# Kernel optimization log

Measured on AMD Instinct MI355X. Metric: run time of the kernel, lower is better.

Reference implementation:

```python
import jax, jax.numpy as jnp
import numpy as np

H = 768
NH = 12
HD = H // NH

def _layernorm(x, g, b, eps=1e-5):
    mu = jnp.mean(x, axis=-1, keepdims=True)
    var = jnp.var(x, axis=-1, keepdims=True)
    return (x - mu) * jax.lax.rsqrt(var + eps) * g + b

def setup_inputs() -> dict:
    key = jax.random.key(0)
    ks = jax.random.split(key, 16)
    s = 0.02
    inp = {
        "x": jax.random.normal(ks[0], (2, 2048, H), jnp.float32),
        "t": jax.random.normal(ks[1], (2, 1, H), jnp.float32),
        # MHA params
        "w_qkv": jax.random.normal(ks[2], (H, 3 * H), jnp.float32) * s,
        "b_qkv": jnp.zeros((3 * H,), jnp.float32),
        "w_mffn1": jax.random.normal(ks[3], (H, 4 * H), jnp.float32) * s,
        "b_mffn1": jnp.zeros((4 * H,), jnp.float32),
        "w_mffn2": jax.random.normal(ks[4], (4 * H, H), jnp.float32) * s,
        "b_mffn2": jnp.zeros((H,), jnp.float32),
        # scale_shift (adaLN) params
        "w_ss1": jax.random.normal(ks[5], (H, 6 * H), jnp.float32) * s,
        "b_ss1": jnp.zeros((6 * H,), jnp.float32),
        "w_ss2": jax.random.normal(ks[6], (6 * H, 6 * H), jnp.float32) * s,
        "b_ss2": jnp.zeros((6 * H,), jnp.float32),
        # layernorms
        "ln1_g": jnp.ones((H,), jnp.float32),
        "ln1_b": jnp.zeros((H,), jnp.float32),
        "ln2_g": jnp.ones((H,), jnp.float32),
        "ln2_b": jnp.zeros((H,), jnp.float32),
        # DiT block FFN
        "w_ffn1": jax.random.normal(ks[7], (H, 4 * H), jnp.float32) * s,
        "b_ffn1": jnp.zeros((4 * H,), jnp.float32),
        "w_ffn2": jax.random.normal(ks[8], (4 * H, H), jnp.float32) * s,
        "b_ffn2": jnp.zeros((H,), jnp.float32),
    }
    return inp

def _mha(x, w_qkv, b_qkv, w1, b1, w2, b2):
    B, T, _ = x.shape
    qkv = x @ w_qkv + b_qkv                      # [B,T,3H]
    qkv = qkv.reshape(B, T, 3, NH, HD)           # split (n h s) as in rearrange
    q, k, v = [jnp.transpose(qkv[:, :, i], (0, 2, 1, 3)) for i in range(3)]  # [B,NH,T,HD]
    # NOTE: faithful to source: scale by 1/sqrt(hidden_size), not head_dim
    wei = jnp.einsum('bhtd,bhsd->bhts', q, k) / jnp.sqrt(jnp.asarray(H, x.dtype))
    wei = jax.nn.softmax(wei, axis=-1)           # [B,NH,T,T] (dropout p=0)
    o = jnp.einsum('bhts,bhsd->bhtd', wei, v)    # [B,NH,T,HD]
    o = jnp.transpose(o, (0, 2, 1, 3)).reshape(B, T, H)
    o = jax.nn.gelu(o @ w1 + b1, approximate=False) @ w2 + b2
    return o

def reference(x, t, w_qkv, b_qkv, w_mffn1, b_mffn1, w_mffn2, b_mffn2,
              w_ss1, b_ss1, w_ss2, b_ss2, ln1_g, ln1_b, ln2_g, ln2_b,
              w_ffn1, b_ffn1, w_ffn2, b_ffn2):
    t_emb = jax.nn.silu(t @ w_ss1 + b_ss1) @ w_ss2 + b_ss2   # [B,1,6H]
    g1, be1, a1, g2, be2, a2 = jnp.split(t_emb, 6, axis=-1)  # each [B,1,H]
    residual = x
    h = g1 * _layernorm(x, ln1_g, ln1_b) + be1
    h = _mha(h, w_qkv, b_qkv, w_mffn1, b_mffn1, w_mffn2, b_mffn2)
    x = residual + a1 * h
    residual = x
    h = g2 * _layernorm(x, ln2_g, ln2_b) + be2
    h = jax.nn.gelu(h @ w_ffn1 + b_ffn1, approximate=False) @ w_ffn2 + b_ffn2
    x = residual + a2 * h
    return x
```

## Files before the change

kernel.cpp:

```cpp
#include <hip/hip_runtime.h>
#include <hip/hip_bf16.h>
#include <cstdint>

typedef __bf16 bf16x8 __attribute__((ext_vector_type(8)));
typedef float f32x4 __attribute__((ext_vector_type(4)));

#define SCALE_Q_LOG2E 0.052058770734702875f

__device__ inline float fast_exp2(float x) { return __builtin_amdgcn_exp2f(x); }

struct PrepArgs {
  const float* src[5];
  __hip_bfloat16* dst[5];
  int K[5], N[5];
  int start[6];
  const float* tin;
  const float* w_ss1;
  float* tacc1;
};

__global__ void k_prep(PrepArgs pa) {
  __shared__ float tile[32][33];
  int bid = blockIdx.x;
  int tid = threadIdx.x;
  if (bid < pa.start[5]) {
    int i = 0;
#pragma unroll
    for (int j = 1; j < 5; ++j)
      if (bid >= pa.start[j]) i = j;
    int t0 = bid - pa.start[i];
    int N = pa.N[i], K = pa.K[i];
    int ntx = N >> 5;
    int bx = t0 % ntx, by = t0 / ntx;
    const float* src = pa.src[i];
    __hip_bfloat16* dst = pa.dst[i];
    int n0 = bx * 32, k0 = by * 32;
    int tx = tid & 31, ty = tid >> 5;
#pragma unroll
    for (int r = 0; r < 32; r += 8)
      tile[ty + r][tx] = src[(size_t)(k0 + ty + r) * N + n0 + tx];
    __syncthreads();
#pragma unroll
    for (int r = 0; r < 32; r += 8)
      dst[(size_t)(n0 + ty + r) * K + k0 + tx] = __float2bfloat16(tile[tx][ty + r]);
  } else {
    int t0 = bid - pa.start[5];
    int nb = t0 % 18, kb0 = (t0 / 18) * 64;
    int n = nb * 256 + tid;
    float a0 = 0.f, a1 = 0.f;
    for (int k = kb0; k < kb0 + 64; ++k) {
      float w = pa.w_ss1[(size_t)k * 4608 + n];
      a0 += pa.tin[k] * w;
      a1 += pa.tin[768 + k] * w;
    }
    atomicAdd(&pa.tacc1[n], a0);
    atomicAdd(&pa.tacc1[4608 + n], a1);
  }
}

__global__ void k_tvec2_silu(const float* __restrict__ tacc1, const float* __restrict__ bss1,
                             const float* __restrict__ W, float* __restrict__ teacc) {
  int n = blockIdx.x * 256 + threadIdx.x;
  int kb = blockIdx.y * 64;
  float a0 = 0.f, a1 = 0.f;
  for (int k = kb; k < kb + 64; ++k) {
    float w = W[(size_t)k * 4608 + n];
    float bs = bss1[k];
    float t0 = tacc1[k] + bs;
    float t1 = tacc1[4608 + k] + bs;
    t0 = t0 / (1.f + expf(-t0));
    t1 = t1 / (1.f + expf(-t1));
    a0 += t0 * w;
    a1 += t1 * w;
  }
  atomicAdd(&teacc[n], a0);
  atomicAdd(&teacc[4608 + n], a1);
}

__global__ void k_ln_mod(const float* __restrict__ x, const float* __restrict__ lng,
                         const float* __restrict__ lnb, const float* __restrict__ teacc,
                         const float* __restrict__ bss2,
                         int gofs, int bofs, __hip_bfloat16* __restrict__ out) {
  int row = blockIdx.x;
  int b = row >> 11;
  const float* xr = x + (size_t)row * 768;
  int tid = threadIdx.x;
  float v[3];
  float s = 0.f, sq = 0.f;
#pragma unroll
  for (int i = 0; i < 3; ++i) { v[i] = xr[tid + 256 * i]; s += v[i]; sq += v[i] * v[i]; }
#pragma unroll
  for (int o = 32; o > 0; o >>= 1) { s += __shfl_xor(s, o); sq += __shfl_xor(sq, o); }
  __shared__ float rs[4], rq[4];
  int w = tid >> 6, lane = tid & 63;
  if (lane == 0) { rs[w] = s; rq[w] = sq; }
  __syncthreads();
  s = rs[0] + rs[1] + rs[2] + rs[3];
  sq = rq[0] + rq[1] + rq[2] + rq[3];
  float mu = s * (1.f / 768.f);
  float var = sq * (1.f / 768.f) - mu * mu;
  float rstd = rsqrtf(var + 1e-5f);
  const float* tb = teacc + (size_t)b * 4608;
#pragma unroll
  for (int i = 0; i < 3; ++i) {
    int n = tid + 256 * i;
    float gv = tb[gofs + n] + bss2[gofs + n];
    float bv = tb[bofs + n] + bss2[bofs + n];
    float h = (v[i] - mu) * rstd * lng[n] + lnb[n];
    h = gv * h + bv;
    out[(size_t)row * 768 + n] = __float2bfloat16(h);
  }
}

template <int BM, int BN, int EPI>
__global__ __launch_bounds__(256)
void k_gemm(const __hip_bfloat16* __restrict__ A,
            const __hip_bfloat16* __restrict__ Bt,
            const float* __restrict__ bias,
            float* __restrict__ outF, __hip_bfloat16* __restrict__ outB,
            __hip_bfloat16* __restrict__ outV,
            const float* __restrict__ res, const float* __restrict__ teacc,
            const float* __restrict__ bss2,
            int gofs, int M, int N, int K) {
  constexpr int MI = BM / 32;
  constexpr int NI = BN / 32;
  __shared__ __align__(16) __hip_bfloat16 As[BM * 64];
  __shared__ __align__(16) __hip_bfloat16 Bs[BN * 64];
  const int tid = threadIdx.x;
  const int w = tid >> 6, lane = tid & 63;
  const int quad = lane >> 4, l16 = lane & 15;
  const int wm = w & 1, wn = w >> 1;
  const int m0 = blockIdx.y * BM, n0 = blockIdx.x * BN;
  const int srow = lane >> 3;
  const int sco = ((lane & 7) ^ srow) * 8;

  f32x4 acc[MI][NI] = {};

  for (int k0 = 0; k0 < K; k0 += 64) {
#pragma unroll
    for (int ii = 0; ii < BM / 32; ++ii) {
      int is = w * (BM / 32) + ii;
      const __hip_bfloat16* g = A + (size_t)(m0 + is * 8 + srow) * K + k0 + sco;
      __builtin_amdgcn_global_load_lds(
          (const __attribute__((address_space(1))) void*)g,
          (__attribute__((address_space(3))) void*)&As[is * 512], 16, 0, 0);
    }
#pragma unroll
    for (int ii = 0; ii < BN / 32; ++ii) {
      int is = w * (BN / 32) + ii;
      const __hip_bfloat16* g = Bt + (size_t)(n0 + is * 8 + srow) * K + k0 + sco;
      __builtin_amdgcn_global_load_lds(
          (const __attribute__((address_space(1))) void*)g,
          (__attribute__((address_space(3))) void*)&Bs[is * 512], 16, 0, 0);
    }
    __syncthreads();
#pragma unroll
    for (int ks = 0; ks < 2; ++ks) {
      bf16x8 af[MI], bfv[NI];
#pragma unroll
      for (int i = 0; i < MI; ++i) {
        int row = wm * (BM / 2) + i * 16 + l16;
        int cph = (ks * 4 + quad) ^ (row & 7);
        af[i] = *(const bf16x8*)&As[row * 64 + cph * 8];
      }
#pragma unroll
      for (int j = 0; j < NI; ++j) {
        int row = wn * (BN / 2) + j * 16 + l16;
        int cph = (ks * 4 + quad) ^ (row & 7);
        bfv[j] = *(const bf16x8*)&Bs[row * 64 + cph * 8];
      }
#pragma unroll
      for (int i = 0; i < MI; ++i)
#pragma unroll
        for (int j = 0; j < NI; ++j)
          acc[i][j] = __builtin_amdgcn_mfma_f32_16x16x32_bf16(af[i], bfv[j], acc[i][j], 0, 0, 0);
    }
    __syncthreads();
  }

#pragma unroll
  for (int j = 0; j < NI; ++j) {
    int col = n0 + wn * (BN / 2) + j * 16 + l16;
    float bs = bias[col];
#pragma unroll
    for (int i = 0; i < MI; ++i) {
      int row0 = m0 + wm * (BM / 2) + i * 16 + quad * 4;
      if (EPI == 3 && col >= 1536) {
        int d = col - 1536;
        int nh = d >> 6, dl = d & 63;
        int bb = row0 >> 11, tok = row0 & 2047;
        __hip_bfloat16 tmp[4];
#pragma unroll
        for (int r = 0; r < 4; ++r) tmp[r] = __float2bfloat16(acc[i][j][r] + bs);
        *(uint2*)&outV[((size_t)(bb * 12 + nh) * 64 + dl) * 2048 + tok] = *(uint2*)tmp;
      } else {
#pragma unroll
        for (int r = 0; r < 4; ++r) {
          int row = row0 + r;
          float v = acc[i][j][r] + bs;
          size_t idx = (size_t)row * N + col;
          if (EPI == 0) {
            outF[idx] = v;
          } else if (EPI == 1) {
            float v2 = v * v;
            float u = v * (0.79788456080286536f + 0.035677408136300125f * v2);
            float e = fast_exp2(u * 2.8853900817779268f);
            float gl = v - v * __builtin_amdgcn_rcpf(e + 1.f);
            outB[idx] = __float2bfloat16(gl);
          } else if (EPI == 2) {
            float gate = teacc[(size_t)(row >> 11) * 4608 + gofs + col] + bss2[gofs + col];
            outF[idx] = res[idx] + gate * v;
          } else {
            float vq = (col < 768) ? v * SCALE_Q_LOG2E : v;
            outB[idx] = __float2bfloat16(vq);
          }
        }
      }
    }
  }
}

__launch_bounds__(256)
__global__ void k_attn(const __hip_bfloat16* __restrict__ qkvb,
                       const __hip_bfloat16* __restrict__ VT,
                       __hip_bfloat16* __restrict__ out) {
  __shared__ __align__(16) __hip_bfloat16 Ks[128 * 64];
  __shared__ __align__(16) __hip_bfloat16 Vs[64 * 128];
  __shared__ __align__(16) __hip_bfloat16 Pw[4][16 * 128];

  const int tid = threadIdx.x;
  const int w = tid >> 6, lane = tid & 63;
  const int quad = lane >> 4, l16 = lane & 15;
  const int qt = blockIdx.x, nh = blockIdx.y, b = blockIdx.z;
  const int bh = b * 12 + nh;

  const int qrow0 = b * 2048 + qt * 64 + w * 16;
  bf16x8 qf[2];
#pragma unroll
  for (int t = 0; t < 2; ++t)
    qf[t] = *(const bf16x8*)(qkvb + (size_t)(qrow0 + l16) * 2304 + nh * 64 + t * 32 + quad * 8);

  bf16x8 ones;
#pragma unroll
  for (int j = 0; j < 8; ++j) ones[j] = (__bf16)1.0f;

  f32x4 o[4] = {};
  f32x4 o_l = {};

  const int srow8 = lane >> 3;
  const int sco8 = ((lane & 7) ^ srow8) * 8;
  const int srow4 = lane >> 4;

  for (int kt = 0; kt < 16; ++kt) {
    __syncthreads();
#pragma unroll
    for (int ii = 0; ii < 4; ++ii) {
      int i = w * 4 + ii;
      const __hip_bfloat16* gk =
          qkvb + (size_t)(b * 2048 + kt * 128 + i * 8 + srow8) * 2304 + 768 + nh * 64 + sco8;
      __builtin_amdgcn_global_load_lds(
          (const __attribute__((address_space(1))) void*)gk,
          (__attribute__((address_space(3))) void*)&Ks[i * 512], 16, 0, 0);
      int vrow = i * 4 + srow4;
      const __hip_bfloat16* gv =
          VT + (size_t)(bh * 64 + vrow) * 2048 + kt * 128 + (((lane & 15) ^ (vrow & 15)) * 8);
      __builtin_amdgcn_global_load_lds(
          (const __attribute__((address_space(1))) void*)gv,
          (__attribute__((address_space(3))) void*)&Vs[i * 512], 16, 0, 0);
    }
    __syncthreads();

    f32x4 s_acc[8] = {};
#pragma unroll
    for (int t = 0; t < 2; ++t) {
#pragma unroll
      for (int c = 0; c < 8; ++c) {
        int row = c * 16 + l16;
        int cph = (t * 4 + quad) ^ (row & 7);
        bf16x8 kf = *(const bf16x8*)&Ks[row * 64 + cph * 8];
        s_acc[c] = __builtin_amdgcn_mfma_f32_16x16x32_bf16(qf[t], kf, s_acc[c], 0, 0, 0);
      }
    }

#pragma unroll
    for (int c = 0; c < 8; ++c) {
      int chunk = c * 2 + (l16 >> 3);
#pragma unroll
      for (int r = 0; r < 4; ++r) {
        float p = fast_exp2(s_acc[c][r]);
        int row = quad * 4 + r;
        int phys = chunk ^ row;
        Pw[w][row * 128 + phys * 8 + (l16 & 7)] = __float2bfloat16(p);
      }
    }

#pragma unroll
    for (int t2 = 0; t2 < 4; ++t2) {
      int phys_p = ((t2 * 4 + quad) ^ l16);
      bf16x8 pa = *(const bf16x8*)&Pw[w][l16 * 128 + phys_p * 8];
#pragma unroll
      for (int nf = 0; nf < 4; ++nf) {
        int row = nf * 16 + l16;
        int cph = (t2 * 4 + quad) ^ (row & 15);
        bf16x8 vf = *(const bf16x8*)&Vs[row * 128 + cph * 8];
        o[nf] = __builtin_amdgcn_mfma_f32_16x16x32_bf16(pa, vf, o[nf], 0, 0, 0);
      }
      o_l = __builtin_amdgcn_mfma_f32_16x16x32_bf16(pa, ones, o_l, 0, 0, 0);
    }
  }

  {
    float inv[4];
#pragma unroll
    for (int r = 0; r < 4; ++r) inv[r] = 1.f / o_l[r];
#pragma unroll
    for (int nf = 0; nf < 4; ++nf)
#pragma unroll
      for (int r = 0; r < 4; ++r) {
        int row = qrow0 + quad * 4 + r;
        out[(size_t)row * 768 + nh * 64 + nf * 16 + l16] = __float2bfloat16(o[nf][r] * inv[r]);
      }
  }
}

extern "C" void kernel_launch(void* const* d_in, const int* in_sizes, int n_in,
                              void* d_out, int out_size, void* d_ws, size_t ws_size,
                              hipStream_t stream) {
  const float* x      = (const float*)d_in[0];
  const float* t      = (const float*)d_in[1];
  const float* w_qkv  = (const float*)d_in[2];
  const float* b_qkv  = (const float*)d_in[3];
  const float* w_m1   = (const float*)d_in[4];
  const float* b_m1   = (const float*)d_in[5];
  const float* w_m2   = (const float*)d_in[6];
  const float* b_m2   = (const float*)d_in[7];
  const float* w_ss1  = (const float*)d_in[8];
  const float* b_ss1  = (const float*)d_in[9];
  const float* w_ss2  = (const float*)d_in[10];
  const float* b_ss2  = (const float*)d_in[11];
  const float* ln1_g  = (const float*)d_in[12];
  const float* ln1_b  = (const float*)d_in[13];
  const float* ln2_g  = (const float*)d_in[14];
  const float* ln2_b  = (const float*)d_in[15];
  const float* w_f1   = (const float*)d_in[16];
  const float* b_f1   = (const float*)d_in[17];
  const float* w_f2   = (const float*)d_in[18];
  const float* b_f2   = (const float*)d_in[19];
  float* out = (float*)d_out;

  char* ws = (char*)d_ws;
  size_t off = 0;
  auto alloc = [&](size_t bytes) -> char* {
    off = (off + 255) & ~(size_t)255;
    char* p = ws + off;
    off += bytes;
    return p;
  };
  __hip_bfloat16* wtq  = (__hip_bfloat16*)alloc((size_t)2304 * 768 * 2);
  __hip_bfloat16* wtm1 = (__hip_bfloat16*)alloc((size_t)3072 * 768 * 2);
  __hip_bfloat16* wtm2 = (__hip_bfloat16*)alloc((size_t)768 * 3072 * 2);
  __hip_bfloat16* wtf1 = (__hip_bfloat16*)alloc((size_t)3072 * 768 * 2);
  __hip_bfloat16* wtf2 = (__hip_bfloat16*)alloc((size_t)768 * 3072 * 2);
  float* tacc1 = (float*)alloc(9216 * 4);
  float* teacc = (float*)alloc(9216 * 4);
  __hip_bfloat16* h1   = (__hip_bfloat16*)alloc((size_t)4096 * 768 * 2);
  __hip_bfloat16* qkvb = (__hip_bfloat16*)alloc((size_t)4096 * 2304 * 2);
  __hip_bfloat16* VT   = (__hip_bfloat16*)alloc((size_t)24 * 64 * 2048 * 2);
  __hip_bfloat16* attn = (__hip_bfloat16*)alloc((size_t)4096 * 768 * 2);
  __hip_bfloat16* act1 = (__hip_bfloat16*)alloc((size_t)4096 * 3072 * 2);
  float* x1            = (float*)alloc((size_t)4096 * 768 * 4);

  (void)hipMemsetAsync(tacc1, 0, 9216 * 4, stream);
  (void)hipMemsetAsync(teacc, 0, 9216 * 4, stream);

  PrepArgs pa;
  pa.src[0] = w_qkv; pa.dst[0] = wtq;  pa.K[0] = 768;  pa.N[0] = 2304;
  pa.src[1] = w_m1;  pa.dst[1] = wtm1; pa.K[1] = 768;  pa.N[1] = 3072;
  pa.src[2] = w_m2;  pa.dst[2] = wtm2; pa.K[2] = 3072; pa.N[2] = 768;
  pa.src[3] = w_f1;  pa.dst[3] = wtf1; pa.K[3] = 768;  pa.N[3] = 3072;
  pa.src[4] = w_f2;  pa.dst[4] = wtf2; pa.K[4] = 3072; pa.N[4] = 768;
  pa.start[0] = 0;
  pa.start[1] = pa.start[0] + (2304 / 32) * (768 / 32);
  pa.start[2] = pa.start[1] + (3072 / 32) * (768 / 32);
  pa.start[3] = pa.start[2] + (768 / 32) * (3072 / 32);
  pa.start[4] = pa.start[3] + (3072 / 32) * (768 / 32);
  pa.start[5] = pa.start[4] + (768 / 32) * (3072 / 32);
  pa.tin = t; pa.w_ss1 = w_ss1; pa.tacc1 = tacc1;
  int tvec1_blocks = 18 * 12;
  k_prep<<<pa.start[5] + tvec1_blocks, 256, 0, stream>>>(pa);

  k_tvec2_silu<<<dim3(4608 / 256, 4608 / 64), 256, 0, stream>>>(tacc1, b_ss1, w_ss2, teacc);

  k_ln_mod<<<4096, 256, 0, stream>>>(x, ln1_g, ln1_b, teacc, b_ss2, 0, 768, h1);
  k_gemm<64, 128, 3><<<dim3(2304 / 128, 4096 / 64), 256, 0, stream>>>(
      h1, wtq, b_qkv, nullptr, qkvb, VT, nullptr, nullptr, nullptr, 0, 4096, 2304, 768);
  k_attn<<<dim3(32, 12, 2), 256, 0, stream>>>(qkvb, VT, attn);
  k_gemm<128, 128, 1><<<dim3(3072 / 128, 4096 / 128), 256, 0, stream>>>(
      attn, wtm1, b_m1, nullptr, act1, nullptr, nullptr, nullptr, nullptr, 0, 4096, 3072, 768);
  k_gemm<64, 128, 2><<<dim3(768 / 128, 4096 / 64), 256, 0, stream>>>(
      act1, wtm2, b_m2, x1, nullptr, nullptr, x, teacc, b_ss2, 1536, 4096, 768, 3072);

  k_ln_mod<<<4096, 256, 0, stream>>>(x1, ln2_g, ln2_b, teacc, b_ss2, 2304, 3072, h1);
  k_gemm<128, 128, 1><<<dim3(3072 / 128, 4096 / 128), 256, 0, stream>>>(
      h1, wtf1, b_f1, nullptr, act1, nullptr, nullptr, nullptr, nullptr, 0, 4096, 3072, 768);
  k_gemm<64, 128, 2><<<dim3(768 / 128, 4096 / 64), 256, 0, stream>>>(
      act1, wtf2, b_f2, out, nullptr, nullptr, x1, teacc, b_ss2, 3840, 4096, 768, 3072);
}
```

Measured before the change: 483.4 us.

## Double-buffer K tiles in attention and reuse K buffer for P

The attention kernel now prefetches the next K tile into a second LDS buffer while the current tile is being computed. V is still loaded each iteration but is waited on separately through fine-grained vmcnt counts and raw s_barrier calls, so the V load overlaps the QK^T MFMAs. The separate P scratch array is removed, and P is written into the consumed K buffer, which keeps LDS use roughly flat. It also raises wave priority around the MFMA sections with s_setprio. The risk is that the hand-written waitcnt counts must exactly match the number of outstanding loads, or the kernel reads stale data.

```diff
diff --git a/kernel.cpp b/kernel.cpp
--- a/kernel.cpp
+++ b/kernel.cpp
@@ -224,9 +224,8 @@
 __global__ void k_attn(const __hip_bfloat16* __restrict__ qkvb,
                        const __hip_bfloat16* __restrict__ VT,
                        __hip_bfloat16* __restrict__ out) {
-  __shared__ __align__(16) __hip_bfloat16 Ks[128 * 64];
+  __shared__ __align__(16) __hip_bfloat16 Ks[2][128 * 64];
   __shared__ __align__(16) __hip_bfloat16 Vs[64 * 128];
-  __shared__ __align__(16) __hip_bfloat16 Pw[4][16 * 128];
 
   const int tid = threadIdx.x;
   const int w = tid >> 6, lane = tid & 63;
@@ -239,6 +238,7 @@
 #pragma unroll
   for (int t = 0; t < 2; ++t)
     qf[t] = *(const bf16x8*)(qkvb + (size_t)(qrow0 + l16) * 2304 + nh * 64 + t * 32 + quad * 8);
+  asm volatile("s_waitcnt vmcnt(0)" ::: "memory");
 
   bf16x8 ones;
 #pragma unroll
@@ -251,16 +251,26 @@
   const int sco8 = ((lane & 7) ^ srow8) * 8;
   const int srow4 = lane >> 4;
 
+#pragma unroll
+  for (int ii = 0; ii < 4; ++ii) {
+    int i = w * 4 + ii;
+    const __hip_bfloat16* gk =
+        qkvb + (size_t)(b * 2048 + i * 8 + srow8) * 2304 + 768 + nh * 64 + sco8;
+    __builtin_amdgcn_global_load_lds(
+        (const __attribute__((address_space(1))) void*)gk,
+        (__attribute__((address_space(3))) void*)&Ks[0][i * 512], 16, 0, 0);
+  }
+
+#pragma unroll 1
   for (int kt = 0; kt < 16; ++kt) {
-    __syncthreads();
+    const int cur = kt & 1;
+
+    asm volatile("s_waitcnt lgkmcnt(0)" ::: "memory");
+    __builtin_amdgcn_s_barrier();
+
 #pragma unroll
     for (int ii = 0; ii < 4; ++ii) {
       int i = w * 4 + ii;
-      const __hip_bfloat16* gk =
-          qkvb + (size_t)(b * 2048 + kt * 128 + i * 8 + srow8) * 2304 + 768 + nh * 64 + sco8;
-      __builtin_amdgcn_global_load_lds(
-          (const __attribute__((address_space(1))) void*)gk,
-          (__attribute__((address_space(3))) void*)&Ks[i * 512], 16, 0, 0);
       int vrow = i * 4 + srow4;
       const __hip_bfloat16* gv =
           VT + (size_t)(bh * 64 + vrow) * 2048 + kt * 128 + (((lane & 15) ^ (vrow & 15)) * 8);
@@ -268,20 +278,40 @@
           (const __attribute__((address_space(1))) void*)gv,
           (__attribute__((address_space(3))) void*)&Vs[i * 512], 16, 0, 0);
     }
-    __syncthreads();
+    if (kt < 15) {
+#pragma unroll
+      for (int ii = 0; ii < 4; ++ii) {
+        int i = w * 4 + ii;
+        const __hip_bfloat16* gk =
+            qkvb + (size_t)(b * 2048 + (kt + 1) * 128 + i * 8 + srow8) * 2304 + 768 + nh * 64 + sco8;
+        __builtin_amdgcn_global_load_lds(
+            (const __attribute__((address_space(1))) void*)gk,
+            (__attribute__((address_space(3))) void*)&Ks[cur ^ 1][i * 512], 16, 0, 0);
+      }
+      asm volatile("s_waitcnt vmcnt(8)" ::: "memory");
+    } else {
+      asm volatile("s_waitcnt vmcnt(4)" ::: "memory");
+    }
+    __builtin_amdgcn_s_barrier();
 
     f32x4 s_acc[8] = {};
+    __builtin_amdgcn_s_setprio(1);
 #pragma unroll
     for (int t = 0; t < 2; ++t) {
 #pragma unroll
       for (int c = 0; c < 8; ++c) {
         int row = c * 16 + l16;
         int cph = (t * 4 + quad) ^ (row & 7);
-        bf16x8 kf = *(const bf16x8*)&Ks[row * 64 + cph * 8];
+        bf16x8 kf = *(const bf16x8*)&Ks[cur][row * 64 + cph * 8];
         s_acc[c] = __builtin_amdgcn_mfma_f32_16x16x32_bf16(qf[t], kf, s_acc[c], 0, 0, 0);
       }
     }
-
+    __builtin_amdgcn_s_setprio(0);
+
+    asm volatile("s_waitcnt lgkmcnt(0)" ::: "memory");
+    __builtin_amdgcn_s_barrier();
+
+    __hip_bfloat16* Pb = &Ks[cur][w * 2048];
 #pragma unroll
     for (int c = 0; c < 8; ++c) {
       int chunk = c * 2 + (l16 >> 3);
@@ -290,14 +320,20 @@
         float p = fast_exp2(s_acc[c][r]);
         int row = quad * 4 + r;
         int phys = chunk ^ row;
-        Pw[w][row * 128 + phys * 8 + (l16 & 7)] = __float2bfloat16(p);
-      }
-    }
-
+        Pb[row * 128 + phys * 8 + (l16 & 7)] = __float2bfloat16(p);
+      }
+    }
+
+    if (kt < 15) asm volatile("s_waitcnt vmcnt(4)" ::: "memory");
+    else         asm volatile("s_waitcnt vmcnt(0)" ::: "memory");
+    asm volatile("s_waitcnt lgkmcnt(0)" ::: "memory");
+    __builtin_amdgcn_s_barrier();
+
+    __builtin_amdgcn_s_setprio(1);
 #pragma unroll
     for (int t2 = 0; t2 < 4; ++t2) {
       int phys_p = ((t2 * 4 + quad) ^ l16);
-      bf16x8 pa = *(const bf16x8*)&Pw[w][l16 * 128 + phys_p * 8];
+      bf16x8 pa = *(const bf16x8*)&Pb[l16 * 128 + phys_p * 8];
 #pragma unroll
       for (int nf = 0; nf < 4; ++nf) {
         int row = nf * 16 + l16;
@@ -307,6 +343,7 @@
       }
       o_l = __builtin_amdgcn_mfma_f32_16x16x32_bf16(pa, ones, o_l, 0, 0, 0);
     }
+    __builtin_amdgcn_s_setprio(0);
   }
 
   {
```

After: 500.8 us. +3.6%, slower.
